# Optimization experiments

Measured on AMD Instinct MI355X. Metric: run time of the kernel, lower is better.

The kernel has to match this reference:

```python
import jax, jax.numpy as jnp
import numpy as np

N = 50000      # particles (nodes)
E = 300000     # contacts (directed edges), avg degree 6
H = 128        # hidden_features
L = 6          # num_hidden_layers
GF = 12        # graph (global) feature dim: domain(3)+t(1)+x_global(4)+domain_next(3)+t_next(1)
NG = 1         # number of graphs in batch
SP, SV, SW = 1e-3, 1e-3, 1e-2   # scale_position, scale_velocity, scale_angular_velocity
IN_EMB = GF + 1 + 6              # 19 : r + v + globals
IN_MSG = 2 * H + 3 + 6 + 2 + GF  # 279: h_i,h_j,dpos,dv,r_i,r_j,globals
IN_UPD = 2 * H + GF              # 268: h, aggregated message, globals


def _lin_params(key, fan_in, fan_out):
    k1, k2 = jax.random.split(key)
    s = 1.0 / np.sqrt(fan_in)
    W = jax.random.uniform(k1, (fan_in, fan_out), jnp.float32, -s, s)
    b = jax.random.uniform(k2, (fan_out,), jnp.float32, -s, s)
    return W, b


def setup_inputs() -> dict:
    key = jax.random.key(0)
    ks = jax.random.split(key, 40)
    inp = {}
    inp['v'] = jax.random.normal(ks[0], (N, 6), jnp.float32) * 0.01
    inp['pos'] = jax.random.uniform(ks[1], (N, 3), jnp.float32)
    inp['r'] = jax.random.uniform(ks[2], (N, 1), jnp.float32) * 0.05 + 0.01
    inp['domain'] = jnp.ones((3,), jnp.float32)
    inp['t'] = jnp.full((1,), 0.5, jnp.float32)
    inp['x_global'] = jax.random.normal(ks[3], (4,), jnp.float32)
    inp['domain_next'] = jnp.ones((3,), jnp.float32)
    inp['t_next'] = jnp.full((1,), 0.6, jnp.float32)
    inp['edge_index'] = jax.random.randint(ks[4], (2, E), 0, N, jnp.int32)
    inp['batch'] = jnp.zeros((N,), jnp.int32)
    inp['emb_W1'], inp['emb_b1'] = _lin_params(ks[5], IN_EMB, H)
    inp['emb_W2'], inp['emb_b2'] = _lin_params(ks[6], H, H)
    mw1, mb1, mw2, mb2, uw1, ub1, uw2, ub2 = ([] for _ in range(8))
    for l in range(L):
        W, b = _lin_params(ks[7 + l], IN_MSG, H); mw1.append(W); mb1.append(b)
        W, b = _lin_params(ks[13 + l], H, H);     mw2.append(W); mb2.append(b)
        W, b = _lin_params(ks[19 + l], IN_UPD, H); uw1.append(W); ub1.append(b)
        W, b = _lin_params(ks[25 + l], H, H);     uw2.append(W); ub2.append(b)
    inp['msg_W1'] = jnp.stack(mw1); inp['msg_b1'] = jnp.stack(mb1)
    inp['msg_W2'] = jnp.stack(mw2); inp['msg_b2'] = jnp.stack(mb2)
    inp['upd_W1'] = jnp.stack(uw1); inp['upd_b1'] = jnp.stack(ub1)
    inp['upd_W2'] = jnp.stack(uw2); inp['upd_b2'] = jnp.stack(ub2)
    inp['out_W1'], inp['out_b1'] = _lin_params(ks[31], H, H)
    inp['out_W2'], inp['out_b2'] = _lin_params(ks[32], H, 9)
    inp['mac_W1'], inp['mac_b1'] = _lin_params(ks[33], H, H)
    inp['mac_W2'], inp['mac_b2'] = _lin_params(ks[34], H, 3)
    return inp


def _instance_norm(h, batch):
    # per-graph, per-channel normalization over nodes (PyG InstanceNorm, affine=False)
    cnt = jax.ops.segment_sum(jnp.ones((h.shape[0],), h.dtype), batch, NG)[:, None]
    mean = jax.ops.segment_sum(h, batch, NG) / cnt
    d = h - mean[batch]
    var = jax.ops.segment_sum(d * d, batch, NG) / cnt
    return d / jnp.sqrt(var[batch] + 1e-5)


def reference(v, pos, r, domain, t, x_global, domain_next, t_next, edge_index, batch,
              emb_W1, emb_b1, emb_W2, emb_b2,
              msg_W1, msg_b1, msg_W2, msg_b2,
              upd_W1, upd_b1, upd_W2, upd_b2,
              out_W1, out_b1, out_W2, out_b2,
              mac_W1, mac_b1, mac_W2, mac_b2):
    gf = jnp.concatenate((domain, t, x_global, domain_next, t_next))   # [12]
    gfN = jnp.broadcast_to(gf, (v.shape[0], gf.shape[0]))
    node_features = jnp.concatenate((pos, v), axis=1)                  # [N,9]
    feat = jnp.concatenate((r, v, gfN), axis=1)                        # [N,19]
    h = jax.nn.relu(jax.nn.relu(feat @ emb_W1 + emb_b1) @ emb_W2 + emb_b2)
    src, dst = edge_index[0], edge_index[1]
    ones_e = jnp.ones((src.shape[0],), h.dtype)
    deg = jnp.maximum(jax.ops.segment_sum(ones_e, dst, v.shape[0]), 1.0)[:, None]
    gfE = jnp.broadcast_to(gf, (src.shape[0], gf.shape[0]))
    for l in range(L):
        dpos = pos[dst] - pos[src]
        dpos = dpos - domain * jnp.round(dpos / domain)                # periodic minimum image
        m_in = jnp.concatenate((h[dst], h[src], dpos, v[dst] - v[src], r[dst], r[src], gfE), axis=1)
        m = jax.nn.relu(jax.nn.relu(m_in @ msg_W1[l] + msg_b1[l]) @ msg_W2[l] + msg_b2[l])
        agg = jax.ops.segment_sum(m, dst, v.shape[0]) / deg            # mean aggregation
        u_in = jnp.concatenate((h, agg, gfN), axis=1)
        upd = jax.nn.relu(u_in @ upd_W1[l] + upd_b1[l]) @ upd_W2[l] + upd_b2[l]
        h = _instance_norm(h + upd, batch)                             # residual + InstanceNorm
    out = jax.nn.relu(h @ out_W1 + out_b1) @ out_W2 + out_b2           # [N,9]
    scaled = jnp.concatenate((SP * out[:, :3], SV * out[:, 3:6], SW * out[:, 6:]), axis=1)
    pred = scaled + node_features
    pred_x = jnp.remainder(pred[:, :3], domain_next)
    pred_v = pred[:, 3:]
    cnt = jax.ops.segment_sum(jnp.ones((h.shape[0],), h.dtype), batch, NG)[:, None]
    h_mean = jax.ops.segment_sum(h, batch, NG) / cnt                   # global mean pool
    pred_macro = (jax.nn.relu(h_mean @ mac_W1 + mac_b1) @ mac_W2 + mac_b2)[0]
    return (pred_x, pred_v, pred_macro)
```

## Files before the change

kernel.cpp:

```cpp
#include <hip/hip_runtime.h>

#define NNODES 50000
#define NEDGES 300000
#define NL 6
#define AP 132

typedef float f32x4 __attribute__((ext_vector_type(4)));
typedef short s16x8 __attribute__((ext_vector_type(8)));
typedef unsigned short u16x4 __attribute__((ext_vector_type(4)));

#define MFMA(A,B,C) __builtin_amdgcn_mfma_f32_16x16x32_bf16((A),(B),(C),0,0,0)

__device__ __forceinline__ unsigned short bf_hi(float x){
  unsigned u = __float_as_uint(x);
  u += 0x7fffu + ((u>>16)&1u);
  return (unsigned short)(u>>16);
}
__device__ __forceinline__ float bf_f(unsigned short s){
  return __uint_as_float(((unsigned)s)<<16);
}
__device__ __forceinline__ void split2(float x, unsigned short &h, unsigned short &l){
  h = bf_hi(x);
  l = bf_hi(x - bf_f(h));
}

__device__ __forceinline__ f32x4 mm3(s16x8 ah, s16x8 al, s16x8 bh, s16x8 bl, f32x4 c){
  c = MFMA(ah, bh, c);
  c = MFMA(ah, bl, c);
  c = MFMA(al, bh, c);
  return c;
}

__device__ __forceinline__ void pack_tile(const float* W, int K, const float* iv,
                                          unsigned short* dst, int kt, int nt, int lane){
  int col = nt*16 + (lane&15);
  int k0 = kt*32 + (lane>>4)*8;
  s16x8 hv, lv;
  #pragma unroll
  for(int j=0;j<8;j++){
    int k = k0 + j;
    float x = 0.f;
    if(k < K){
      x = W[(size_t)k*128 + col];
      if(iv) x *= iv[k];
    }
    unsigned short hh, ll; split2(x, hh, ll);
    hv[j] = (short)hh; lv[j] = (short)ll;
  }
  unsigned short* p = dst + ((size_t)((kt<<3)+nt)*64 + lane)*16;
  *(s16x8*)p = hv;
  *(s16x8*)(p+8) = lv;
}
__device__ __forceinline__ void ld_b(const unsigned short* P, int kt, int nt, int lane,
                                     s16x8 &bh, s16x8 &bl){
  const unsigned short* p = P + ((size_t)((kt<<3)+nt)*64 + lane)*16;
  bh = *(const s16x8*)p;
  bl = *(const s16x8*)(p+8);
}
__device__ __forceinline__ s16x8 ld_z(const unsigned short* z, int row, int kByte){
  return *(const s16x8*)((const char*)z + row*256 + (kByte ^ ((row&7)<<4)));
}
__device__ __forceinline__ void st_z(unsigned short* zH, unsigned short* zL, int row, int col, float x){
  unsigned short hh, ll; split2(x, hh, ll);
  int byte = row*256 + ((col*2) ^ ((row&7)<<4));
  *(unsigned short*)((char*)zH + byte) = hh;
  *(unsigned short*)((char*)zL + byte) = ll;
}
__device__ __forceinline__ s16x8 ld_t(const unsigned short* z, int row, int kByte){
  return *(const s16x8*)((const char*)z + row*64 + (kByte ^ ((row&3)<<4)));
}

__global__ void k_gf(const float* dom, const float* t, const float* xg,
                     const float* domn, const float* tn, float* gf){
  int i = threadIdx.x;
  if(i < 3)        gf[i]  = dom[i];
  else if(i == 3)  gf[3]  = t[0];
  else if(i < 8)   gf[i]  = xg[i-4];
  else if(i < 11)  gf[i]  = domn[i-8];
  else if(i == 11) gf[11] = tn[0];
}

__global__ void k_deg(const int* ei, float* deg){
  int e = blockIdx.x*blockDim.x + threadIdx.x;
  if(e < NEDGES) atomicAdd(&deg[ei[NEDGES + e]], 1.0f);
}

__global__ void k_histi(const int* ei, int* cnt){
  int e = blockIdx.x*blockDim.x + threadIdx.x;
  if(e < NEDGES) atomicAdd(&cnt[ei[NEDGES + e]], 1);
}

__global__ __launch_bounds__(1024) void k_scan(const int* cnt, int* off){
  __shared__ int buf[1024];
  __shared__ int carry;
  int t = threadIdx.x;
  if(t == 0) carry = 0;
  __syncthreads();
  for(int base = 0; base < NNODES; base += 1024){
    int i = base + t;
    int x = (i < NNODES) ? cnt[i] : 0;
    buf[t] = x;
    __syncthreads();
    for(int ofs = 1; ofs < 1024; ofs <<= 1){
      int y = (t >= ofs) ? buf[t-ofs] : 0;
      __syncthreads();
      buf[t] += y;
      __syncthreads();
    }
    if(i < NNODES) off[i] = carry + buf[t] - x;
    __syncthreads();
    if(t == 1023) carry += buf[1023];
    __syncthreads();
  }
  if(t == 0) off[NNODES] = carry;
}

__global__ void k_scatter(const int* ei, const int* off, int* cur, int* srcP, int* dstP){
  int e = blockIdx.x*blockDim.x + threadIdx.x;
  if(e < NEDGES){
    int s = ei[e], d = ei[NEDGES + e];
    int p = atomicAdd(&cur[d], 1);
    int ix = off[d] + p;
    srcP[ix] = s; dstP[ix] = d;
  }
}

__global__ void k_gfb(const float* gf, const float* mW1, const float* mB1, float* bb1){
  int i = blockIdx.x*256 + threadIdx.x;
  if(i < 768){
    int l = i >> 7, c = i & 127;
    float s = mB1[l*128 + c];
    #pragma unroll
    for(int j=0;j<12;j++) s = fmaf(gf[j], mW1[(size_t)l*35712 + (size_t)(267+j)*128 + c], s);
    bb1[i] = s;
  }
}

__global__ void k_gfb2(const float* gf, const float* mW1, const float* mB1,
                       const float* uW1, const float* uB1, float* bb1s, float* ub1s){
  int i = blockIdx.x*256 + threadIdx.x;
  if(i < 768){
    int l = i>>7, c = i&127;
    float s = mB1[l*128+c];
    #pragma unroll
    for(int j=0;j<12;j++) s = fmaf(gf[j], mW1[(size_t)l*35712 + (size_t)(267+j)*128 + c], s);
    bb1s[i] = s;
  } else if(i < 1536){
    int i2 = i-768, l = i2>>7, c = i2&127;
    float s = uB1[l*128+c];
    #pragma unroll
    for(int j=0;j<12;j++) s = fmaf(gf[j], uW1[(size_t)l*34304 + (size_t)(256+j)*128 + c], s);
    ub1s[i2] = s;
  }
}

__global__ void k_fold(const float* S, float* muiv, int l){
  int c = threadIdx.x;
  if(c >= 128) return;
  if(l == 0){ muiv[c] = 0.f; muiv[128+c] = 1.f; return; }
  float mean = S[c] * (1.0f/NNODES);
  float var  = S[128+c] * (1.0f/NNODES) - mean*mean;
  if(var < 0.f) var = 0.f;
  muiv[c] = mean;
  muiv[128+c] = rsqrtf(var + 1e-5f);
}

__global__ void k_dynbias(const float* muiv, const float* bb1s, const float* ub1s,
                          const float* msgW1l, const float* updW1l,
                          float* bb1d, float* ub1d){
  int c = threadIdx.x;
  if(blockIdx.x == 0){
    float s = bb1s[c];
    for(int k=0;k<128;k++){
      float f = muiv[k]*muiv[128+k];
      s -= f*(msgW1l[(size_t)k*128+c] + msgW1l[(size_t)(128+k)*128+c]);
    }
    bb1d[c] = s;
  } else {
    float s = ub1s[c];
    for(int k=0;k<128;k++) s -= muiv[k]*muiv[128+k]*updW1l[(size_t)k*128+c];
    ub1d[c] = s;
  }
}

__global__ void k_packAll(const float* msgW1, const float* msgW2,
                          const float* updW1, const float* updW2,
                          unsigned short* mPedge, unsigned short* mPw2,
                          unsigned short* uPagg, unsigned short* uPw2){
  int b = blockIdx.x, lane = threadIdx.x;
  if(b < 192){
    int l=b/32, t=b%32;
    pack_tile(msgW2 + (size_t)l*16384, 128, 0, mPw2 + (size_t)l*32768, t/8, t%8, lane);
  } else if(b < 384){
    int bb=b-192, l=bb/32, t=bb%32;
    pack_tile(updW1 + (size_t)l*34304 + 16384, 128, 0, uPagg + (size_t)l*32768, t/8, t%8, lane);
  } else if(b < 576){
    int bb=b-384, l=bb/32, t=bb%32;
    pack_tile(updW2 + (size_t)l*16384, 128, 0, uPw2 + (size_t)l*32768, t/8, t%8, lane);
  } else {
    int bb=b-576, l=bb/8, nt=bb%8;
    pack_tile(msgW1 + (size_t)l*35712 + 32768, 11, 0, mPedge + (size_t)l*8192, 0, nt, lane);
  }
}

__global__ void k_packDyn(const float* msgW1l, const float* updW1l, const float* muiv,
                          unsigned short* mPdst, unsigned short* mPsrc, unsigned short* uPh){
  int b = blockIdx.x, lane = threadIdx.x;
  const float* iv = muiv + 128;
  if(b < 32) pack_tile(msgW1l, 128, iv, mPdst, b>>3, b&7, lane);
  else if(b < 64){ int t=b-32; pack_tile(msgW1l + 16384, 128, iv, mPsrc, t>>3, t&7, lane); }
  else { int t=b-64; pack_tile(updW1l, 128, iv, uPh, t>>3, t&7, lane); }
}

__device__ __forceinline__ void fill_w(float* sW, const float* gW, int KC){
  for(int idx = threadIdx.x; idx < 32*32; idx += 256){
    int kk = idx >> 5, c4 = (idx & 31)*4;
    float4 w = make_float4(0.f,0.f,0.f,0.f);
    if(kk < KC) w = *(const float4*)(gW + (size_t)kk*128 + c4);
    *(float4*)(sW + kk*128 + c4) = w;
  }
}
__device__ __forceinline__ void gemm_chunk(const float* At, const float* sW,
                                           int KCp, int rg, int jc, float acc[4][4]){
  for(int kkg = 0; kkg < KCp; kkg += 4){
    float4 av[4];
    #pragma unroll
    for(int i=0;i<4;i++) av[i] = *(const float4*)(At + (rg*4+i)*AP + kkg);
    #pragma unroll
    for(int q=0;q<4;q++){
      float4 bq = *(const float4*)(sW + (kkg+q)*128 + 4*jc);
      #pragma unroll
      for(int i=0;i<4;i++){
        float aa = ((const float*)&av[i])[q];
        acc[i][0] = fmaf(aa, bq.x, acc[i][0]);
        acc[i][1] = fmaf(aa, bq.y, acc[i][1]);
        acc[i][2] = fmaf(aa, bq.z, acc[i][2]);
        acc[i][3] = fmaf(aa, bq.w, acc[i][3]);
      }
    }
  }
}
__device__ __forceinline__ void gemm_phase(const float* sA, float* sW, const float* gW,
                                           int K, int rg, int jc, float acc[4][4]){
  for(int k0 = 0; k0 < K; k0 += 32){
    int KC = (K - k0 < 32) ? (K - k0) : 32;
    __syncthreads();
    fill_w(sW, gW + (size_t)k0*128, KC);
    __syncthreads();
    gemm_chunk(sA + k0, sW, (KC+3)&~3, rg, jc, acc);
  }
}
__device__ __forceinline__ void init_bias(float acc[4][4], const float* b, int jc){
  float4 bb = *(const float4*)(b + 4*jc);
  #pragma unroll
  for(int i=0;i<4;i++){ acc[i][0]=bb.x; acc[i][1]=bb.y; acc[i][2]=bb.z; acc[i][3]=bb.w; }
}

__global__ __launch_bounds__(256) void k_embed(const float* r, const float* v, const float* gf,
    const float* W1, const float* b1, const float* W2, const float* b2, float* h,
    unsigned short* hPu){
  __shared__ __align__(16) float sA[32*AP];
  __shared__ __align__(16) float sW[32*128];
  __shared__ float sGf[12];
  int t = threadIdx.x, n0 = blockIdx.x*32;
  if(t < 12) sGf[t] = gf[t];
  __syncthreads();
  for(int idx = t; idx < 32*20; idx += 256){
    int row = idx/20, c = idx%20;
    int n = n0 + row; if(n >= NNODES) n = NNODES-1;
    float val;
    if(c == 0)      val = r[n];
    else if(c < 7)  val = v[(size_t)n*6 + (c-1)];
    else if(c < 19) val = sGf[c-7];
    else            val = 0.0f;
    sA[row*AP + c] = val;
  }
  int rg = t>>5, jc = t&31;
  float acc[4][4];
  init_bias(acc, b1, jc);
  gemm_phase(sA, sW, W1, 19, rg, jc, acc);
  __syncthreads();
  #pragma unroll
  for(int i=0;i<4;i++){
    float4 x = make_float4(fmaxf(acc[i][0],0.f), fmaxf(acc[i][1],0.f),
                           fmaxf(acc[i][2],0.f), fmaxf(acc[i][3],0.f));
    *(float4*)&sA[(rg*4+i)*AP + 4*jc] = x;
  }
  init_bias(acc, b2, jc);
  gemm_phase(sA, sW, W2, 128, rg, jc, acc);
  #pragma unroll
  for(int i=0;i<4;i++){
    int n = n0 + rg*4 + i;
    if(n < NNODES){
      float4 x = make_float4(fmaxf(acc[i][0],0.f), fmaxf(acc[i][1],0.f),
                             fmaxf(acc[i][2],0.f), fmaxf(acc[i][3],0.f));
      *(float4*)&h[(size_t)n*128 + 4*jc] = x;
      if(hPu){
        unsigned short h0,h1,h2,h3,l0,l1,l2,l3;
        split2(x.x,h0,l0); split2(x.y,h1,l1); split2(x.z,h2,l2); split2(x.w,h3,l3);
        u16x4 hv; hv[0]=h0; hv[1]=h1; hv[2]=h2; hv[3]=h3;
        u16x4 lv; lv[0]=l0; lv[1]=l1; lv[2]=l2; lv[3]=l3;
        *(u16x4*)&hPu[(size_t)n*256 + 4*jc] = hv;
        *(u16x4*)&hPu[(size_t)n*256 + 128 + 4*jc] = lv;
      }
    }
  }
}

__global__ __launch_bounds__(256) void k_msgM2(const int* __restrict__ srcP, const int* __restrict__ dstP,
    const unsigned short* __restrict__ hPu,
    const float* __restrict__ pos, const float* __restrict__ v, const float* __restrict__ r,
    const float* __restrict__ dom,
    const unsigned short* __restrict__ mPdst, const unsigned short* __restrict__ mPsrc,
    const unsigned short* __restrict__ mPedge, const unsigned short* __restrict__ mPw2,
    const float* __restrict__ bb1d, const float* __restrict__ b2, float* __restrict__ agg)
{
  __shared__ __align__(16) unsigned short zBuf[16384];
  __shared__ __align__(16) unsigned short sTh[2048], sTl[2048];
  __shared__ int sSrc[64], sDst[64];
  __shared__ float sDom[3];
  unsigned short* zH = zBuf;
  unsigned short* zL = zBuf + 8192;
  int t = threadIdx.x;
  int bid = blockIdx.x;
  int swz = (bid & 7)*586 + (bid >> 3);
  int e0 = swz*64;
  int evalid = NEDGES - e0; if(evalid > 64) evalid = 64;
  int w = t>>6, lane = t&63, lr = lane&15, g = lane>>4;
  int nt0 = w*2, nt1 = nt0+1;
  if(t < 64){
    int ee = e0 + t; if(ee >= NEDGES) ee = NEDGES-1;
    sSrc[t] = srcP[ee]; sDst[t] = dstP[ee];
  }
  if(t >= 64 && t < 67) sDom[t-64] = dom[t-64];
  {
    s16x8 zz = {0,0,0,0,0,0,0,0};
    ((s16x8*)sTh)[t] = zz;
    ((s16x8*)sTl)[t] = zz;
  }
  __syncthreads();
  if(t < 64){
    int s = sSrc[t], d = sDst[t];
    float f[11];
    #pragma unroll
    for(int c=0;c<3;c++){
      float dp = pos[(size_t)d*3+c] - pos[(size_t)s*3+c];
      float dm = sDom[c];
      f[c] = dp - dm*rintf(dp/dm);
    }
    #pragma unroll
    for(int c=0;c<6;c++) f[3+c] = v[(size_t)d*6+c] - v[(size_t)s*6+c];
    f[9] = r[d]; f[10] = r[s];
    #pragma unroll
    for(int k=0;k<11;k++){
      unsigned short hh, ll; split2(f[k], hh, ll);
      int byte = t*64 + ((k*2) ^ ((t&3)<<4));
      *(unsigned short*)((char*)sTh + byte) = hh;
      *(unsigned short*)((char*)sTl + byte) = ll;
    }
  }
  float bias0 = bb1d[nt0*16+lr], bias1 = bb1d[nt1*16+lr];
  f32x4 A0[4], A1[4];
  #pragma unroll
  for(int rt=0;rt<4;rt++){
    f32x4 b0 = {bias0,bias0,bias0,bias0};
    f32x4 b1v = {bias1,bias1,bias1,bias1};
    A0[rt] = b0; A1[rt] = b1v;
  }
  __syncthreads();
  const unsigned short* pd[4];
  const unsigned short* ps[4];
  #pragma unroll
  for(int rt=0;rt<4;rt++){
    pd[rt] = hPu + (size_t)sDst[rt*16+lr]*256;
    ps[rt] = hPu + (size_t)sSrc[rt*16+lr]*256;
  }
  int ko = g*8;
  #pragma unroll
  for(int kt=0;kt<4;kt++){
    int o = kt*32 + ko;
    s16x8 DH[4], DL[4], SH[4], SL[4];
    #pragma unroll
    for(int rt=0;rt<4;rt++){
      DH[rt] = *(const s16x8*)(pd[rt] + o);
      DL[rt] = *(const s16x8*)(pd[rt] + 128 + o);
      SH[rt] = *(const s16x8*)(ps[rt] + o);
      SL[rt] = *(const s16x8*)(ps[rt] + 128 + o);
    }
    s16x8 bh, bl;
    ld_b(mPdst, kt, nt0, lane, bh, bl);
    #pragma unroll
    for(int rt=0;rt<4;rt++) A0[rt] = mm3(DH[rt], DL[rt], bh, bl, A0[rt]);
    ld_b(mPdst, kt, nt1, lane, bh, bl);
    #pragma unroll
    for(int rt=0;rt<4;rt++) A1[rt] = mm3(DH[rt], DL[rt], bh, bl, A1[rt]);
    ld_b(mPsrc, kt, nt0, lane, bh, bl);
    #pragma unroll
    for(int rt=0;rt<4;rt++) A0[rt] = mm3(SH[rt], SL[rt], bh, bl, A0[rt]);
    ld_b(mPsrc, kt, nt1, lane, bh, bl);
    #pragma unroll
    for(int rt=0;rt<4;rt++) A1[rt] = mm3(SH[rt], SL[rt], bh, bl, A1[rt]);
  }
  {
    s16x8 TH[4], TL[4];
    #pragma unroll
    for(int rt=0;rt<4;rt++){
      TH[rt] = ld_t(sTh, rt*16+lr, g*16);
      TL[rt] = ld_t(sTl, rt*16+lr, g*16);
    }
    s16x8 bh, bl;
    ld_b(mPedge, 0, nt0, lane, bh, bl);
    #pragma unroll
    for(int rt=0;rt<4;rt++) A0[rt] = mm3(TH[rt], TL[rt], bh, bl, A0[rt]);
    ld_b(mPedge, 0, nt1, lane, bh, bl);
    #pragma unroll
    for(int rt=0;rt<4;rt++) A1[rt] = mm3(TH[rt], TL[rt], bh, bl, A1[rt]);
  }
  #pragma unroll
  for(int rt=0;rt<4;rt++){
    #pragma unroll
    for(int i=0;i<4;i++){
      int row = rt*16 + g*4 + i;
      st_z(zH, zL, row, nt0*16+lr, fmaxf(A0[rt][i],0.f));
      st_z(zH, zL, row, nt1*16+lr, fmaxf(A1[rt][i],0.f));
    }
  }
  __syncthreads();
  float c0 = b2[nt0*16+lr], c1 = b2[nt1*16+lr];
  f32x4 M0[4], M1[4];
  #pragma unroll
  for(int rt=0;rt<4;rt++){
    f32x4 b0 = {c0,c0,c0,c0};
    f32x4 b1v = {c1,c1,c1,c1};
    M0[rt] = b0; M1[rt] = b1v;
  }
  #pragma unroll
  for(int kt=0;kt<4;kt++){
    int kb = kt*64 + g*16;
    s16x8 ZHv[4], ZLv[4];
    #pragma unroll
    for(int rt=0;rt<4;rt++){
      ZHv[rt] = ld_z(zH, rt*16+lr, kb);
      ZLv[rt] = ld_z(zL, rt*16+lr, kb);
    }
    s16x8 bh, bl;
    ld_b(mPw2, kt, nt0, lane, bh, bl);
    #pragma unroll
    for(int rt=0;rt<4;rt++) M0[rt] = mm3(ZHv[rt], ZLv[rt], bh, bl, M0[rt]);
    ld_b(mPw2, kt, nt1, lane, bh, bl);
    #pragma unroll
    for(int rt=0;rt<4;rt++) M1[rt] = mm3(ZHv[rt], ZLv[rt], bh, bl, M1[rt]);
  }
  __syncthreads();
  float* sM = (float*)zBuf;
  #pragma unroll
  for(int rt=0;rt<4;rt++){
    #pragma unroll
    for(int i=0;i<4;i++){
      int row = rt*16 + g*4 + i;
      sM[row*128 + nt0*16+lr] = fmaxf(M0[rt][i],0.f);
      sM[row*128 + nt1*16+lr] = fmaxf(M1[rt][i],0.f);
    }
  }
  __syncthreads();
  int col = t & 127, half = t >> 7;
  int rbeg = half*32, rend = rbeg + 32;
  int cur = sDst[rbeg];
  float run = 0.f;
  for(int row = rbeg; row < rend; row++){
    if(row < evalid) run += sM[row*128 + col];
    int nxt = (row+1 < rend) ? sDst[row+1] : -1;
    if(nxt != cur){
      atomicAdd(&agg[(size_t)cur*128 + col], run);
      run = 0.f; cur = nxt;
    }
  }
}

__global__ __launch_bounds__(256) void k_updM(float* __restrict__ h, unsigned short* __restrict__ hPu,
    float* __restrict__ agg, const int* __restrict__ cnt, const float* __restrict__ muiv,
    const unsigned short* __restrict__ uPh, const unsigned short* __restrict__ uPagg,
    const unsigned short* __restrict__ uPw2,
    const float* __restrict__ ub1d, const float* __restrict__ b2, float* __restrict__ S)
{
  __shared__ __align__(16) unsigned short zBuf[8192];
  __shared__ __align__(16) float sH[32*AP];
  __shared__ float sRd[32];
  __shared__ float stS[512], stQ[512];
  unsigned short* zH = zBuf; unsigned short* zL = zBuf + 4096;
  int t = threadIdx.x, n0 = blockIdx.x*32;
  int w = t>>6, lane = t&63, lr = lane&15, g = lane>>4;
  int nt0 = w*2, nt1 = nt0+1;
  if(t < 32){
    int n = n0 + t; if(n >= NNODES) n = NNODES-1;
    sRd[t] = 1.0f / fmaxf((float)cnt[n], 1.0f);
  }
  __syncthreads();
  for(int idx = t; idx < 1024; idx += 256){
    int row = idx>>5, c4 = (idx&31)*4;
    int n = n0 + row; bool valid = (n < NNODES); if(!valid) n = NNODES-1;
    float4 hx = *(const float4*)&h[(size_t)n*128 + c4];
    *(float4*)&sH[row*AP + c4] = hx;
    float4 ax = *(const float4*)&agg[(size_t)n*128 + c4];
    float rd = sRd[row];
    ax.x*=rd; ax.y*=rd; ax.z*=rd; ax.w*=rd;
    unsigned short h0,h1,h2,h3,l0,l1,l2,l3;
    split2(ax.x,h0,l0); split2(ax.y,h1,l1); split2(ax.z,h2,l2); split2(ax.w,h3,l3);
    int byte = row*256 + ((c4*2) ^ ((row&7)<<4));
    u16x4 hv; hv[0]=h0; hv[1]=h1; hv[2]=h2; hv[3]=h3;
    u16x4 lv; lv[0]=l0; lv[1]=l1; lv[2]=l2; lv[3]=l3;
    *(u16x4*)((char*)zH + byte) = hv;
    *(u16x4*)((char*)zL + byte) = lv;
    if(valid) *(float4*)&agg[(size_t)n*128 + c4] = make_float4(0.f,0.f,0.f,0.f);
  }
  __syncthreads();
  float bias0 = ub1d[nt0*16+lr], bias1 = ub1d[nt1*16+lr];
  f32x4 a00 = {bias0,bias0,bias0,bias0};
  f32x4 a01 = {bias1,bias1,bias1,bias1};
  f32x4 a10 = a00, a11 = a01;
  int nA0 = n0+lr;    if(nA0 >= NNODES) nA0 = NNODES-1;
  int nA1 = n0+16+lr; if(nA1 >= NNODES) nA1 = NNODES-1;
  const unsigned short* ph0 = hPu + (size_t)nA0*256;
  const unsigned short* ph1 = hPu + (size_t)nA1*256;
  int ko = g*8;
  #pragma unroll
  for(int kt=0;kt<4;kt++){
    int o = kt*32 + ko;
    s16x8 ah0 = *(const s16x8*)(ph0 + o), al0 = *(const s16x8*)(ph0 + 128 + o);
    s16x8 ah1 = *(const s16x8*)(ph1 + o), al1 = *(const s16x8*)(ph1 + 128 + o);
    s16x8 bh, bl;
    ld_b(uPh, kt, nt0, lane, bh, bl);
    a00 = mm3(ah0, al0, bh, bl, a00);
    a10 = mm3(ah1, al1, bh, bl, a10);
    ld_b(uPh, kt, nt1, lane, bh, bl);
    a01 = mm3(ah0, al0, bh, bl, a01);
    a11 = mm3(ah1, al1, bh, bl, a11);
    int kb = kt*64 + g*16;
    s16x8 gh0 = ld_z(zH, lr, kb),    gl0 = ld_z(zL, lr, kb);
    s16x8 gh1 = ld_z(zH, 16+lr, kb), gl1 = ld_z(zL, 16+lr, kb);
    ld_b(uPagg, kt, nt0, lane, bh, bl);
    a00 = mm3(gh0, gl0, bh, bl, a00);
    a10 = mm3(gh1, gl1, bh, bl, a10);
    ld_b(uPagg, kt, nt1, lane, bh, bl);
    a01 = mm3(gh0, gl0, bh, bl, a01);
    a11 = mm3(gh1, gl1, bh, bl, a11);
  }
  __syncthreads();
  #pragma unroll
  for(int i=0;i<4;i++){
    int r0 = g*4+i, r1 = 16+g*4+i;
    st_z(zH, zL, r0, nt0*16+lr, fmaxf(a00[i],0.f));
    st_z(zH, zL, r0, nt1*16+lr, fmaxf(a01[i],0.f));
    st_z(zH, zL, r1, nt0*16+lr, fmaxf(a10[i],0.f));
    st_z(zH, zL, r1, nt1*16+lr, fmaxf(a11[i],0.f));
  }
  __syncthreads();
  float c0 = b2[nt0*16+lr], c1 = b2[nt1*16+lr];
  f32x4 m00 = {c0,c0,c0,c0}, m01 = {c1,c1,c1,c1};
  f32x4 m10 = m00, m11 = m01;
  #pragma unroll
  for(int kt=0;kt<4;kt++){
    int kb = kt*64 + g*16;
    s16x8 ah0 = ld_z(zH, lr, kb),    al0 = ld_z(zL, lr, kb);
    s16x8 ah1 = ld_z(zH, 16+lr, kb), al1 = ld_z(zL, 16+lr, kb);
    s16x8 bh, bl;
    ld_b(uPw2, kt, nt0, lane, bh, bl);
    m00 = mm3(ah0, al0, bh, bl, m00);
    m10 = mm3(ah1, al1, bh, bl, m10);
    ld_b(uPw2, kt, nt1, lane, bh, bl);
    m01 = mm3(ah0, al0, bh, bl, m01);
    m11 = mm3(ah1, al1, bh, bl, m11);
  }
  int col0 = nt0*16+lr, col1 = nt1*16+lr;
  float mu0 = muiv[col0], iv0 = muiv[128+col0];
  float mu1 = muiv[col1], iv1 = muiv[128+col1];
  float s0=0.f,q0=0.f,s1=0.f,q1=0.f;
  #pragma unroll
  for(int tm=0;tm<2;tm++){
    #pragma unroll
    for(int i=0;i<4;i++){
      int row = tm*16 + g*4 + i;
      int n = n0 + row;
      if(n < NNODES){
        float acc0 = (tm==0) ? m00[i] : m10[i];
        float acc1 = (tm==0) ? m01[i] : m11[i];
        float v0 = (sH[row*AP+col0]-mu0)*iv0 + acc0;
        float v1 = (sH[row*AP+col1]-mu1)*iv1 + acc1;
        h[(size_t)n*128+col0] = v0;
        h[(size_t)n*128+col1] = v1;
        unsigned short hh,ll;
        split2(v0,hh,ll); hPu[(size_t)n*256+col0]=hh; hPu[(size_t)n*256+128+col0]=ll;
        split2(v1,hh,ll); hPu[(size_t)n*256+col1]=hh; hPu[(size_t)n*256+128+col1]=ll;
        s0+=v0; q0+=v0*v0; s1+=v1; q1+=v1*v1;
      }
    }
  }
  stS[g*128+col0]=s0; stQ[g*128+col0]=q0;
  stS[g*128+col1]=s1; stQ[g*128+col1]=q1;
  __syncthreads();
  if(t < 128){
    float s = stS[t]+stS[128+t]+stS[256+t]+stS[384+t];
    float q = stQ[t]+stQ[128+t]+stQ[256+t]+stQ[384+t];
    atomicAdd(&S[t], s);
    atomicAdd(&S[128 + t], q);
  }
}

__global__ __launch_bounds__(256) void k_pre(const float* h, const float* W1, float* P){
  __shared__ __align__(16) float sA[32*AP];
  __shared__ __align__(16) float sW[32*128];
  int t = threadIdx.x, n0 = blockIdx.x*32;
  for(int idx = t; idx < 1024; idx += 256){
    int row = idx>>5, c4 = (idx&31)*4;
    int n = n0 + row; if(n >= NNODES) n = NNODES-1;
    *(float4*)&sA[row*AP + c4] = *(const float4*)&h[(size_t)n*128 + c4];
  }
  int rg = t>>5, jc = t&31;
  float acc[4][4];
  #pragma unroll
  for(int i=0;i<4;i++){ acc[i][0]=0.f; acc[i][1]=0.f; acc[i][2]=0.f; acc[i][3]=0.f; }
  gemm_phase(sA, sW, W1, 128, rg, jc, acc);
  #pragma unroll
  for(int i=0;i<4;i++){
    int n = n0 + rg*4 + i;
    if(n < NNODES)
      *(float4*)&P[(size_t)n*256 + 4*jc] = make_float4(acc[i][0],acc[i][1],acc[i][2],acc[i][3]);
  }
  #pragma unroll
// ... 152 lines not shown
  }
  __shared__ float ls[256], lq[256];
  ls[threadIdx.x] = s; lq[threadIdx.x] = q;
  __syncthreads();
  if(half == 0){
    atomicAdd(&sum[col], ls[col] + ls[128+col]);
    atomicAdd(&sq[col],  lq[col] + lq[128+col]);
  }
}

__global__ void k_norm(float* h, const float* sum, const float* sq){
  size_t i = (size_t)blockIdx.x*256 + threadIdx.x;
  if(i < (size_t)NNODES*128){
    int col = i & 127;
    float mean = sum[col] * (1.0f/NNODES);
    float var  = sq[col] * (1.0f/NNODES) - mean*mean;
    if(var < 0.f) var = 0.f;
    h[i] = (h[i] - mean) * rsqrtf(var + 1e-5f);
  }
}

__global__ __launch_bounds__(256) void k_out(const float* h, const float* pos, const float* v,
    const float* domn, const float* W1, const float* b1, const float* W2, const float* b2,
    float* out){
  __shared__ __align__(16) float sA[32*AP];
  __shared__ __align__(16) float sW[32*128];
  __shared__ float sW2[128*9], sB2[9], sDn[3];
  int t = threadIdx.x, n0 = blockIdx.x*32;
  for(int idx = t; idx < 128*9; idx += 256) sW2[idx] = W2[idx];
  if(t < 9) sB2[t] = b2[t];
  if(t >= 16 && t < 19) sDn[t-16] = domn[t-16];
  for(int idx = t; idx < 1024; idx += 256){
    int row = idx>>5, c4 = (idx&31)*4;
    int n = n0 + row; if(n >= NNODES) n = NNODES-1;
    *(float4*)&sA[row*AP + c4] = *(const float4*)&h[(size_t)n*128 + c4];
  }
  int rg = t>>5, jc = t&31;
  float acc[4][4];
  init_bias(acc, b1, jc);
  gemm_phase(sA, sW, W1, 128, rg, jc, acc);
  __syncthreads();
  #pragma unroll
  for(int i=0;i<4;i++){
    float4 x = make_float4(fmaxf(acc[i][0],0.f), fmaxf(acc[i][1],0.f),
                           fmaxf(acc[i][2],0.f), fmaxf(acc[i][3],0.f));
    *(float4*)&sA[(rg*4+i)*AP + 4*jc] = x;
  }
  __syncthreads();
  for(int idx = t; idx < 32*9; idx += 256){
    int n = idx/9, c = idx%9;
    int gn = n0 + n;
    if(gn < NNODES){
      float s = sB2[c];
      for(int k=0;k<128;k++) s = fmaf(sA[n*AP + k], sW2[k*9 + c], s);
      if(c < 3){
        float p = 0.001f*s + pos[(size_t)gn*3 + c];
        float dn = sDn[c];
        p = p - floorf(p/dn)*dn;
        out[(size_t)gn*3 + c] = p;
      } else {
        float scale = (c < 6) ? 0.001f : 0.01f;
        float p = scale*s + v[(size_t)gn*6 + (c-3)];
        out[(size_t)150000 + (size_t)gn*6 + (c-3)] = p;
      }
    }
  }
}

__global__ __launch_bounds__(128) void k_macro(const float* sum, const float* W1,
    const float* b1, const float* W2, const float* b2, float* out){
  __shared__ float hm[128], t1[128];
  int t = threadIdx.x;
  hm[t] = sum[t] * (1.0f/NNODES);
  __syncthreads();
  float s = b1[t];
  for(int k=0;k<128;k++) s = fmaf(hm[k], W1[(size_t)k*128 + t], s);
  t1[t] = fmaxf(s, 0.0f);
  __syncthreads();
  if(t < 3){
    float o = b2[t];
    for(int k=0;k<128;k++) o = fmaf(t1[k], W2[(size_t)k*3 + t], o);
    out[450000 + t] = o;
  }
}

extern "C" void kernel_launch(void* const* d_in, const int* in_sizes, int n_in,
                              void* d_out, int out_size, void* d_ws, size_t ws_size,
                              hipStream_t stream){
  const float* v    = (const float*)d_in[0];
  const float* pos  = (const float*)d_in[1];
  const float* r    = (const float*)d_in[2];
  const float* dom  = (const float*)d_in[3];
  const float* tt   = (const float*)d_in[4];
  const float* xg   = (const float*)d_in[5];
  const float* domn = (const float*)d_in[6];
  const float* tn   = (const float*)d_in[7];
  const int*   ei   = (const int*)d_in[8];
  const float* embW1=(const float*)d_in[10]; const float* embB1=(const float*)d_in[11];
  const float* embW2=(const float*)d_in[12]; const float* embB2=(const float*)d_in[13];
  const float* msgW1=(const float*)d_in[14]; const float* msgB1=(const float*)d_in[15];
  const float* msgW2=(const float*)d_in[16]; const float* msgB2=(const float*)d_in[17];
  const float* updW1=(const float*)d_in[18]; const float* updB1=(const float*)d_in[19];
  const float* updW2=(const float*)d_in[20]; const float* updB2=(const float*)d_in[21];
  const float* outW1=(const float*)d_in[22]; const float* outB1=(const float*)d_in[23];
  const float* outW2=(const float*)d_in[24]; const float* outB2=(const float*)d_in[25];
  const float* macW1=(const float*)d_in[26]; const float* macB1=(const float*)d_in[27];
  const float* macW2=(const float*)d_in[28]; const float* macB2=(const float*)d_in[29];

  float* ws = (float*)d_ws;
  float* out = (float*)d_out;
  const bool mf = ws_size >= (size_t)105604292;

  if(mf){
    float* h    = ws;
    float* agg  = ws + (size_t)6400000;
    unsigned short* hPu = (unsigned short*)(ws + 12800000);
    float* Sb   = ws + (size_t)19200000;
    float* gf   = ws + (size_t)19201792;
    float* muiv = ws + (size_t)19201808;
    float* bb1s = ws + (size_t)19202064;
    float* ub1s = ws + (size_t)19202832;
    float* bb1d = ws + (size_t)19203600;
    float* ub1d = ws + (size_t)19203728;
    int* cnt  = (int*)(ws + 19203856);
    int* off  = (int*)(ws + 19253856);
    int* cur  = (int*)(ws + 19303857);
    int* srcP = (int*)(ws + 19353857);
    int* dstP = (int*)(ws + 19653857);
    unsigned short* mPdst  = (unsigned short*)(ws + 19953860);
    unsigned short* mPsrc  = (unsigned short*)(ws + 19970244);
    unsigned short* uPh    = (unsigned short*)(ws + 19986628);
    unsigned short* mPedge = (unsigned short*)(ws + 20003012);
    unsigned short* mPw2   = (unsigned short*)(ws + 20027588);
    unsigned short* uPagg  = (unsigned short*)(ws + 20125892);
    unsigned short* uPw2   = (unsigned short*)(ws + 20224196);

    k_gf<<<1, 64, 0, stream>>>(dom, tt, xg, domn, tn, gf);
    k_gfb2<<<6, 256, 0, stream>>>(gf, msgW1, msgB1, updW1, updB1, bb1s, ub1s);
    k_packAll<<<624, 64, 0, stream>>>(msgW1, msgW2, updW1, updW2, mPedge, mPw2, uPagg, uPw2);
    hipMemsetAsync(Sb, 0, 7*256*4, stream);
    hipMemsetAsync(agg, 0, (size_t)6400000*4, stream);
    hipMemsetAsync(cnt, 0, (size_t)NNODES*4, stream);
    hipMemsetAsync(cur, 0, (size_t)NNODES*4, stream);
    k_histi<<<(NEDGES+255)/256, 256, 0, stream>>>(ei, cnt);
    k_scan<<<1, 1024, 0, stream>>>(cnt, off);
    k_scatter<<<(NEDGES+255)/256, 256, 0, stream>>>(ei, off, cur, srcP, dstP);
    k_embed<<<(NNODES+31)/32, 256, 0, stream>>>(r, v, gf, embW1, embB1, embW2, embB2, h, hPu);
    for(int l = 0; l < NL; l++){
      k_fold<<<1, 128, 0, stream>>>((l > 0) ? (Sb + (l-1)*256) : Sb, muiv, l);
      k_dynbias<<<2, 128, 0, stream>>>(muiv, bb1s + l*128, ub1s + l*128,
          msgW1 + (size_t)l*35712, updW1 + (size_t)l*34304, bb1d, ub1d);
      k_packDyn<<<96, 64, 0, stream>>>(msgW1 + (size_t)l*35712, updW1 + (size_t)l*34304,
          muiv, mPdst, mPsrc, uPh);
      k_msgM2<<<4688, 256, 0, stream>>>(srcP, dstP, hPu, pos, v, r, dom,
          mPdst, mPsrc, mPedge + (size_t)l*8192, mPw2 + (size_t)l*32768,
          bb1d, msgB2 + l*128, agg);
      k_updM<<<(NNODES+31)/32, 256, 0, stream>>>(h, hPu, agg, cnt, muiv,
          uPh, uPagg + (size_t)l*32768, uPw2 + (size_t)l*32768,
          ub1d, updB2 + l*128, Sb + l*256);
    }
    k_norm<<<25000, 256, 0, stream>>>(h, Sb + 5*256, Sb + 5*256 + 128);
    k_stats<<<256, 256, 0, stream>>>(h, Sb + 6*256, Sb + 6*256 + 128);
    k_macro<<<1, 128, 0, stream>>>(Sb + 6*256, macW1, macB1, macW2, macB2, out);
    k_out<<<(NNODES+31)/32, 256, 0, stream>>>(h, pos, v, domn,
                                              outW1, outB1, outW2, outB2, out);
    return;
  }

  float* h   = ws;
  float* agg = ws + (size_t)6400000;
  float* P   = ws + (size_t)12800000;
  float* deg = ws + (size_t)25600000;
  float* gf  = ws + (size_t)25650016;
  float* sum = ws + (size_t)25650048;
  float* sq  = ws + (size_t)25650176;
  float* bb1 = ws + (size_t)25650304;

  k_gf<<<1, 64, 0, stream>>>(dom, tt, xg, domn, tn, gf);
  k_gfb<<<3, 256, 0, stream>>>(gf, msgW1, msgB1, bb1);
  hipMemsetAsync(deg, 0, (size_t)NNODES*4, stream);
  k_deg<<<(NEDGES+255)/256, 256, 0, stream>>>(ei, deg);
  k_embed<<<(NNODES+31)/32, 256, 0, stream>>>(r, v, gf, embW1, embB1, embW2, embB2, h,
                                              (unsigned short*)0);
  for(int l = 0; l < NL; l++){
    hipMemsetAsync(agg, 0, (size_t)6400000*4, stream);
    k_pre<<<(NNODES+31)/32, 256, 0, stream>>>(h, msgW1 + (size_t)l*35712, P);
    k_msg2<<<NEDGES/32, 256, 0, stream>>>(ei, P, pos, v, r, dom,
        msgW1 + (size_t)l*35712, msgW2 + (size_t)l*16384,
        bb1 + l*128, msgB2 + l*128, agg);
    k_upd<<<(NNODES+31)/32, 256, 0, stream>>>(h, agg, deg, gf,
        updW1, updB1, updW2, updB2, l);
    hipMemsetAsync(sum, 0, 128*4, stream);
    hipMemsetAsync(sq,  0, 128*4, stream);
    k_stats<<<256, 256, 0, stream>>>(h, sum, sq);
    k_norm<<<25000, 256, 0, stream>>>(h, sum, sq);
  }
  hipMemsetAsync(sum, 0, 128*4, stream);
  hipMemsetAsync(sq,  0, 128*4, stream);
  k_stats<<<256, 256, 0, stream>>>(h, sum, sq);
  k_macro<<<1, 128, 0, stream>>>(sum, macW1, macB1, macW2, macB2, out);
  k_out<<<(NNODES+31)/32, 256, 0, stream>>>(h, pos, v, domn,
                                            outW1, outB1, outW2, outB2, out);
}
```

Baseline: 1.861 ms.

## Process second-layer message MLP in two 32-row halves to halve LDS

The message kernel's second MLP layer and scatter-add stage now run over two 32-edge halves in sequence, reusing a shared buffer half the previous size. This cuts LDS per block from about 48KB to about 32KB, which can allow more resident blocks per CU. In exchange it adds extra barriers per block and splits the segmented reduction into 16-row runs, which may raise the number of atomics.

```diff
diff --git a/kernel.cpp b/kernel.cpp
--- a/kernel.cpp
+++ b/kernel.cpp
@@ -63,6 +63,15 @@
 __device__ __forceinline__ void st_z(unsigned short* zH, unsigned short* zL, int row, int col, float x){
   unsigned short hh, ll; split2(x, hh, ll);
   int byte = row*256 + ((col*2) ^ ((row&7)<<4));
+  *(unsigned short*)((char*)zH + byte) = hh;
+  *(unsigned short*)((char*)zL + byte) = ll;
+}
+__device__ __forceinline__ s16x8 ld_z2(const unsigned short* z, int row, int kByte){
+  return *(const s16x8*)((const char*)z + (row&31)*256 + (kByte ^ ((row&7)<<4)));
+}
+__device__ __forceinline__ void st_z2(unsigned short* zH, unsigned short* zL, int row, int col, float x){
+  unsigned short hh, ll; split2(x, hh, ll);
+  int byte = (row&31)*256 + ((col*2) ^ ((row&7)<<4));
   *(unsigned short*)((char*)zH + byte) = hh;
   *(unsigned short*)((char*)zL + byte) = ll;
 }
@@ -315,12 +324,12 @@
     const unsigned short* __restrict__ mPedge, const unsigned short* __restrict__ mPw2,
     const float* __restrict__ bb1d, const float* __restrict__ b2, float* __restrict__ agg)
 {
-  __shared__ __align__(16) unsigned short zBuf[16384];
+  __shared__ __align__(16) unsigned short zBuf[8192];
   __shared__ __align__(16) unsigned short sTh[2048], sTl[2048];
   __shared__ int sSrc[64], sDst[64];
   __shared__ float sDom[3];
   unsigned short* zH = zBuf;
-  unsigned short* zL = zBuf + 8192;
+  unsigned short* zL = zBuf + 4096;
   int t = threadIdx.x;
   int bid = blockIdx.x;
   int swz = (bid & 7)*586 + (bid >> 3);
@@ -416,64 +425,70 @@
     #pragma unroll
     for(int rt=0;rt<4;rt++) A1[rt] = mm3(TH[rt], TL[rt], bh, bl, A1[rt]);
   }
-  #pragma unroll
-  for(int rt=0;rt<4;rt++){
-    #pragma unroll
-    for(int i=0;i<4;i++){
-      int row = rt*16 + g*4 + i;
-      st_z(zH, zL, row, nt0*16+lr, fmaxf(A0[rt][i],0.f));
-      st_z(zH, zL, row, nt1*16+lr, fmaxf(A1[rt][i],0.f));
-    }
-  }
-  __syncthreads();
   float c0 = b2[nt0*16+lr], c1 = b2[nt1*16+lr];
-  f32x4 M0[4], M1[4];
-  #pragma unroll
-  for(int rt=0;rt<4;rt++){
-    f32x4 b0 = {c0,c0,c0,c0};
-    f32x4 b1v = {c1,c1,c1,c1};
-    M0[rt] = b0; M1[rt] = b1v;
-  }
-  #pragma unroll
-  for(int kt=0;kt<4;kt++){
-    int kb = kt*64 + g*16;
-    s16x8 ZHv[4], ZLv[4];
-    #pragma unroll
-    for(int rt=0;rt<4;rt++){
-      ZHv[rt] = ld_z(zH, rt*16+lr, kb);
-      ZLv[rt] = ld_z(zL, rt*16+lr, kb);
-    }
-    s16x8 bh, bl;
-    ld_b(mPw2, kt, nt0, lane, bh, bl);
-    #pragma unroll
-    for(int rt=0;rt<4;rt++) M0[rt] = mm3(ZHv[rt], ZLv[rt], bh, bl, M0[rt]);
-    ld_b(mPw2, kt, nt1, lane, bh, bl);
-    #pragma unroll
-    for(int rt=0;rt<4;rt++) M1[rt] = mm3(ZHv[rt], ZLv[rt], bh, bl, M1[rt]);
-  }
-  __syncthreads();
-  float* sM = (float*)zBuf;
-  #pragma unroll
-  for(int rt=0;rt<4;rt++){
-    #pragma unroll
-    for(int i=0;i<4;i++){
-      int row = rt*16 + g*4 + i;
-      sM[row*128 + nt0*16+lr] = fmaxf(M0[rt][i],0.f);
-      sM[row*128 + nt1*16+lr] = fmaxf(M1[rt][i],0.f);
-    }
-  }
-  __syncthreads();
-  int col = t & 127, half = t >> 7;
-  int rbeg = half*32, rend = rbeg + 32;
-  int cur = sDst[rbeg];
-  float run = 0.f;
-  for(int row = rbeg; row < rend; row++){
-    if(row < evalid) run += sM[row*128 + col];
-    int nxt = (row+1 < rend) ? sDst[row+1] : -1;
-    if(nxt != cur){
-      atomicAdd(&agg[(size_t)cur*128 + col], run);
-      run = 0.f; cur = nxt;
-    }
+  #pragma unroll
+  for(int hf=0; hf<2; hf++){
+    #pragma unroll
+    for(int q=0;q<2;q++){
+      int rt = hf*2 + q;
+      #pragma unroll
+      for(int i=0;i<4;i++){
+        int row = rt*16 + g*4 + i;
+        st_z2(zH, zL, row, nt0*16+lr, fmaxf(A0[rt][i],0.f));
+        st_z2(zH, zL, row, nt1*16+lr, fmaxf(A1[rt][i],0.f));
+      }
+    }
+    __syncthreads();
+    f32x4 M0[2], M1[2];
+    #pragma unroll
+    for(int q=0;q<2;q++){
+      f32x4 b0 = {c0,c0,c0,c0};
+      f32x4 b1v = {c1,c1,c1,c1};
+      M0[q] = b0; M1[q] = b1v;
+    }
+    #pragma unroll
+    for(int kt=0;kt<4;kt++){
+      int kb = kt*64 + g*16;
+      s16x8 ZH0 = ld_z2(zH, hf*32 + lr, kb);
+      s16x8 ZL0 = ld_z2(zL, hf*32 + lr, kb);
+      s16x8 ZH1 = ld_z2(zH, hf*32 + 16 + lr, kb);
+      s16x8 ZL1 = ld_z2(zL, hf*32 + 16 + lr, kb);
+      s16x8 bh, bl;
+      ld_b(mPw2, kt, nt0, lane, bh, bl);
+      M0[0] = mm3(ZH0, ZL0, bh, bl, M0[0]);
+      M0[1] = mm3(ZH1, ZL1, bh, bl, M0[1]);
+      ld_b(mPw2, kt, nt1, lane, bh, bl);
+      M1[0] = mm3(ZH0, ZL0, bh, bl, M1[0]);
+      M1[1] = mm3(ZH1, ZL1, bh, bl, M1[1]);
+    }
+    __syncthreads();
+    float* sM = (float*)zBuf;
+    #pragma unroll
+    for(int q=0;q<2;q++){
+      #pragma unroll
+      for(int i=0;i<4;i++){
+        int rloc = q*16 + g*4 + i;
+        sM[rloc*128 + nt0*16+lr] = fmaxf(M0[q][i],0.f);
+        sM[rloc*128 + nt1*16+lr] = fmaxf(M1[q][i],0.f);
+      }
+    }
+    __syncthreads();
+    {
+      int col = t & 127, sub = t >> 7;
+      int rbeg = sub*16, rend = rbeg + 16;
+      int gbase = hf*32;
+      int cur = sDst[gbase + rbeg];
+      float run = 0.f;
+      for(int rr = rbeg; rr < rend; rr++){
+        if(gbase + rr < evalid) run += sM[rr*128 + col];
+        int nxt = (rr+1 < rend) ? sDst[gbase + rr + 1] : -1;
+        if(nxt != cur){
+          atomicAdd(&agg[(size_t)cur*128 + col], run);
+          run = 0.f; cur = nxt;
+        }
+      }
+    }
+    __syncthreads();
   }
 }
 
```

Result: slower. 1.908 ms (+2.5%).

## Restructure message kernel so each wave owns 16 edges across all columns

Applied to the files above, without the earlier changes.

The message MLP kernel is reorganised so each wave computes all 128 output columns for its own 16-edge row tile, instead of splitting columns across waves over all 64 edges. The hidden activation is staged through a small per-wave LDS buffer in two halves, so the block-wide barriers between the two layers and before the scatter are removed. Segmented atomic accumulation is now done straight from registers over 4 rows, and a launch-bounds occupancy hint is added. The trade is that every wave now streams the full weight matrices (4x more B-operand loads per block), and the shorter runs mean more atomics to the aggregation buffer.

```diff
diff --git a/kernel.cpp b/kernel.cpp
--- a/kernel.cpp
+++ b/kernel.cpp
@@ -63,6 +63,15 @@
 __device__ __forceinline__ void st_z(unsigned short* zH, unsigned short* zL, int row, int col, float x){
   unsigned short hh, ll; split2(x, hh, ll);
   int byte = row*256 + ((col*2) ^ ((row&7)<<4));
+  *(unsigned short*)((char*)zH + byte) = hh;
+  *(unsigned short*)((char*)zL + byte) = ll;
+}
+__device__ __forceinline__ s16x8 ld_y(const unsigned short* z, int row, int kByte){
+  return *(const s16x8*)((const char*)z + row*128 + (kByte ^ ((row&7)<<4)));
+}
+__device__ __forceinline__ void st_y(unsigned short* zH, unsigned short* zL, int row, int lcol, float x){
+  unsigned short hh, ll; split2(x, hh, ll);
+  int byte = row*128 + ((lcol*2) ^ ((row&7)<<4));
   *(unsigned short*)((char*)zH + byte) = hh;
   *(unsigned short*)((char*)zL + byte) = ll;
 }
@@ -307,7 +316,7 @@
   }
 }
 
-__global__ __launch_bounds__(256) void k_msgM2(const int* __restrict__ srcP, const int* __restrict__ dstP,
+__global__ __launch_bounds__(256, 4) void k_msgM3(const int* __restrict__ srcP, const int* __restrict__ dstP,
     const unsigned short* __restrict__ hPu,
     const float* __restrict__ pos, const float* __restrict__ v, const float* __restrict__ r,
     const float* __restrict__ dom,
@@ -315,19 +324,16 @@
     const unsigned short* __restrict__ mPedge, const unsigned short* __restrict__ mPw2,
     const float* __restrict__ bb1d, const float* __restrict__ b2, float* __restrict__ agg)
 {
-  __shared__ __align__(16) unsigned short zBuf[16384];
+  __shared__ __align__(16) unsigned short zAll[4][2][1024];
   __shared__ __align__(16) unsigned short sTh[2048], sTl[2048];
   __shared__ int sSrc[64], sDst[64];
   __shared__ float sDom[3];
-  unsigned short* zH = zBuf;
-  unsigned short* zL = zBuf + 8192;
   int t = threadIdx.x;
   int bid = blockIdx.x;
   int swz = (bid & 7)*586 + (bid >> 3);
   int e0 = swz*64;
   int evalid = NEDGES - e0; if(evalid > 64) evalid = 64;
   int w = t>>6, lane = t&63, lr = lane&15, g = lane>>4;
-  int nt0 = w*2, nt1 = nt0+1;
   if(t < 64){
     int ee = e0 + t; if(ee >= NEDGES) ee = NEDGES-1;
     sSrc[t] = srcP[ee]; sDst[t] = dstP[ee];
@@ -359,120 +365,94 @@
       *(unsigned short*)((char*)sTl + byte) = ll;
     }
   }
-  float bias0 = bb1d[nt0*16+lr], bias1 = bb1d[nt1*16+lr];
-  f32x4 A0[4], A1[4];
-  #pragma unroll
-  for(int rt=0;rt<4;rt++){
-    f32x4 b0 = {bias0,bias0,bias0,bias0};
-    f32x4 b1v = {bias1,bias1,bias1,bias1};
-    A0[rt] = b0; A1[rt] = b1v;
-  }
-  __syncthreads();
-  const unsigned short* pd[4];
-  const unsigned short* ps[4];
-  #pragma unroll
-  for(int rt=0;rt<4;rt++){
-    pd[rt] = hPu + (size_t)sDst[rt*16+lr]*256;
-    ps[rt] = hPu + (size_t)sSrc[rt*16+lr]*256;
+  __syncthreads();
+  int erow = (w<<4) + lr;
+  const unsigned short* pd = hPu + (size_t)sDst[erow]*256;
+  const unsigned short* ps = hPu + (size_t)sSrc[erow]*256;
+  f32x4 A[8];
+  #pragma unroll
+  for(int nt=0;nt<8;nt++){
+    float b = bb1d[nt*16+lr];
+    f32x4 bb = {b,b,b,b};
+    A[nt] = bb;
   }
   int ko = g*8;
   #pragma unroll
   for(int kt=0;kt<4;kt++){
     int o = kt*32 + ko;
-    s16x8 DH[4], DL[4], SH[4], SL[4];
-    #pragma unroll
-    for(int rt=0;rt<4;rt++){
-      DH[rt] = *(const s16x8*)(pd[rt] + o);
-      DL[rt] = *(const s16x8*)(pd[rt] + 128 + o);
-      SH[rt] = *(const s16x8*)(ps[rt] + o);
-      SL[rt] = *(const s16x8*)(ps[rt] + 128 + o);
-    }
-    s16x8 bh, bl;
-    ld_b(mPdst, kt, nt0, lane, bh, bl);
-    #pragma unroll
-    for(int rt=0;rt<4;rt++) A0[rt] = mm3(DH[rt], DL[rt], bh, bl, A0[rt]);
-    ld_b(mPdst, kt, nt1, lane, bh, bl);
-    #pragma unroll
-    for(int rt=0;rt<4;rt++) A1[rt] = mm3(DH[rt], DL[rt], bh, bl, A1[rt]);
-    ld_b(mPsrc, kt, nt0, lane, bh, bl);
-    #pragma unroll
-    for(int rt=0;rt<4;rt++) A0[rt] = mm3(SH[rt], SL[rt], bh, bl, A0[rt]);
-    ld_b(mPsrc, kt, nt1, lane, bh, bl);
-    #pragma unroll
-    for(int rt=0;rt<4;rt++) A1[rt] = mm3(SH[rt], SL[rt], bh, bl, A1[rt]);
+    s16x8 DH = *(const s16x8*)(pd + o);
+    s16x8 DL = *(const s16x8*)(pd + 128 + o);
+    s16x8 SH = *(const s16x8*)(ps + o);
+    s16x8 SL = *(const s16x8*)(ps + 128 + o);
+    #pragma unroll
+    for(int nt=0;nt<8;nt++){
+      s16x8 bh, bl;
+      ld_b(mPdst, kt, nt, lane, bh, bl);
+      A[nt] = mm3(DH, DL, bh, bl, A[nt]);
+      ld_b(mPsrc, kt, nt, lane, bh, bl);
+      A[nt] = mm3(SH, SL, bh, bl, A[nt]);
+    }
   }
   {
-    s16x8 TH[4], TL[4];
-    #pragma unroll
-    for(int rt=0;rt<4;rt++){
-      TH[rt] = ld_t(sTh, rt*16+lr, g*16);
-      TL[rt] = ld_t(sTl, rt*16+lr, g*16);
-    }
-    s16x8 bh, bl;
-    ld_b(mPedge, 0, nt0, lane, bh, bl);
-    #pragma unroll
-    for(int rt=0;rt<4;rt++) A0[rt] = mm3(TH[rt], TL[rt], bh, bl, A0[rt]);
-    ld_b(mPedge, 0, nt1, lane, bh, bl);
-    #pragma unroll
-    for(int rt=0;rt<4;rt++) A1[rt] = mm3(TH[rt], TL[rt], bh, bl, A1[rt]);
-  }
-  #pragma unroll
-  for(int rt=0;rt<4;rt++){
+    s16x8 TH = ld_t(sTh, erow, g*16);
+    s16x8 TL = ld_t(sTl, erow, g*16);
+    #pragma unroll
+    for(int nt=0;nt<8;nt++){
+      s16x8 bh, bl;
+      ld_b(mPedge, 0, nt, lane, bh, bl);
+      A[nt] = mm3(TH, TL, bh, bl, A[nt]);
+    }
+  }
+  unsigned short* zH = zAll[w][0];
+  unsigned short* zL = zAll[w][1];
+  f32x4 M[8];
+  #pragma unroll
+  for(int nt=0;nt<8;nt++){
+    float b = b2[nt*16+lr];
+    f32x4 bb = {b,b,b,b};
+    M[nt] = bb;
+  }
+  #pragma unroll
+  for(int hf=0; hf<2; hf++){
+    #pragma unroll
+    for(int q=0;q<4;q++){
+      int nt = hf*4 + q;
+      #pragma unroll
+      for(int i=0;i<4;i++){
+        st_y(zH, zL, g*4+i, q*16+lr, fmaxf(A[nt][i],0.f));
+      }
+    }
+    #pragma unroll
+    for(int kt2=0;kt2<2;kt2++){
+      s16x8 ZH = ld_y(zH, lr, kt2*64 + g*16);
+      s16x8 ZL = ld_y(zL, lr, kt2*64 + g*16);
+      #pragma unroll
+      for(int nt=0;nt<8;nt++){
+        s16x8 bh, bl;
+        ld_b(mPw2, hf*2+kt2, nt, lane, bh, bl);
+        M[nt] = mm3(ZH, ZL, bh, bl, M[nt]);
+      }
+    }
+  }
+  int base = (w<<4) + (g<<2);
+  int dR[4]; bool vR[4];
+  #pragma unroll
+  for(int i=0;i<4;i++){
+    dR[i] = sDst[base+i];
+    vR[i] = (base+i) < evalid;
+  }
+  #pragma unroll
+  for(int nt=0;nt<8;nt++){
+    int col = nt*16 + lr;
+    float run = 0.f; int cur = dR[0];
     #pragma unroll
     for(int i=0;i<4;i++){
-      int row = rt*16 + g*4 + i;
-      st_z(zH, zL, row, nt0*16+lr, fmaxf(A0[rt][i],0.f));
-      st_z(zH, zL, row, nt1*16+lr, fmaxf(A1[rt][i],0.f));
-    }
-  }
-  __syncthreads();
-  float c0 = b2[nt0*16+lr], c1 = b2[nt1*16+lr];
-  f32x4 M0[4], M1[4];
-  #pragma unroll
-  for(int rt=0;rt<4;rt++){
-    f32x4 b0 = {c0,c0,c0,c0};
-    f32x4 b1v = {c1,c1,c1,c1};
-    M0[rt] = b0; M1[rt] = b1v;
-  }
-  #pragma unroll
-  for(int kt=0;kt<4;kt++){
-    int kb = kt*64 + g*16;
-    s16x8 ZHv[4], ZLv[4];
-    #pragma unroll
-    for(int rt=0;rt<4;rt++){
-      ZHv[rt] = ld_z(zH, rt*16+lr, kb);
-      ZLv[rt] = ld_z(zL, rt*16+lr, kb);
-    }
-    s16x8 bh, bl;
-    ld_b(mPw2, kt, nt0, lane, bh, bl);
-    #pragma unroll
-    for(int rt=0;rt<4;rt++) M0[rt] = mm3(ZHv[rt], ZLv[rt], bh, bl, M0[rt]);
-    ld_b(mPw2, kt, nt1, lane, bh, bl);
-    #pragma unroll
-    for(int rt=0;rt<4;rt++) M1[rt] = mm3(ZHv[rt], ZLv[rt], bh, bl, M1[rt]);
-  }
-  __syncthreads();
-  float* sM = (float*)zBuf;
-  #pragma unroll
-  for(int rt=0;rt<4;rt++){
-    #pragma unroll
-    for(int i=0;i<4;i++){
-      int row = rt*16 + g*4 + i;
-      sM[row*128 + nt0*16+lr] = fmaxf(M0[rt][i],0.f);
-      sM[row*128 + nt1*16+lr] = fmaxf(M1[rt][i],0.f);
-    }
-  }
-  __syncthreads();
-  int col = t & 127, half = t >> 7;
-  int rbeg = half*32, rend = rbeg + 32;
-  int cur = sDst[rbeg];
-  float run = 0.f;
-  for(int row = rbeg; row < rend; row++){
-    if(row < evalid) run += sM[row*128 + col];
-    int nxt = (row+1 < rend) ? sDst[row+1] : -1;
-    if(nxt != cur){
-      atomicAdd(&agg[(size_t)cur*128 + col], run);
-      run = 0.f; cur = nxt;
+      if(vR[i]) run += fmaxf(M[nt][i], 0.f);
+      int nxt = (i<3) ? dR[i+1] : -1;
+      if(nxt != cur){
+        atomicAdd(&agg[(size_t)cur*128 + col], run);
+        run = 0.f; cur = nxt;
+      }
     }
   }
 }
@@ -932,7 +912,7 @@
           msgW1 + (size_t)l*35712, updW1 + (size_t)l*34304, bb1d, ub1d);
       k_packDyn<<<96, 64, 0, stream>>>(msgW1 + (size_t)l*35712, updW1 + (size_t)l*34304,
           muiv, mPdst, mPsrc, uPh);
-      k_msgM2<<<4688, 256, 0, stream>>>(srcP, dstP, hPu, pos, v, r, dom,
+      k_msgM3<<<4688, 256, 0, stream>>>(srcP, dstP, hPu, pos, v, r, dom,
           mPdst, mPsrc, mPedge + (size_t)l*8192, mPw2 + (size_t)l*32768,
           bb1d, msgB2 + l*128, agg);
       k_updM<<<(NNODES+31)/32, 256, 0, stream>>>(h, hPu, agg, cnt, muiv,
```

Measured after the change: 2.043 ms. 9.7% more time.
